# Kernel tuning notes

Measured on AMD Instinct MI355X. Metric: run time of the kernel, lower is better.

The kernel has to match this reference:

```python
import math
import jax, jax.numpy as jnp
import numpy as np

N_HEAD = 16
N_GROUPS = 32
EPS = 1e-05


def gelu(x):
    return 0.5 * x * (1.0 + jnp.tanh(math.sqrt(2.0 / math.pi) * (x + 0.044715 * x ** 3)))


def dp_group_norm(x, weight, bias, num_groups=N_GROUPS, eps=EPS):
    # x: [B, T, H]. torch F.group_norm on transposed [B, H, T] normalizes over
    # (channels_per_group, T) jointly per (batch, group).
    B, T, H = x.shape
    xg = x.reshape(B, T, num_groups, H // num_groups)
    mean = jnp.mean(xg, axis=(1, 3), keepdims=True)
    var = jnp.mean((xg - mean) ** 2, axis=(1, 3), keepdims=True)
    xn = ((xg - mean) / jnp.sqrt(var + eps)).reshape(B, T, H)
    return xn * weight + bias


def attention(x, w_attn, b_attn, w_aproj, b_aproj):
    B, T, H = x.shape
    hd = H // N_HEAD
    qkv = x @ w_attn + b_attn                      # [B, T, 3H]
    q, k, v = jnp.split(qkv, 3, axis=-1)
    q = q.reshape(B, T, N_HEAD, hd).transpose(0, 2, 1, 3)   # [B, nh, T, hd]
    k = k.reshape(B, T, N_HEAD, hd).transpose(0, 2, 1, 3)   # [B, nh, T, hd]
    v = v.reshape(B, T, N_HEAD, hd).transpose(0, 2, 1, 3)
    w = jnp.einsum('bhqd,bhkd->bhqk', q, k)        # no 1/sqrt(d): scale=False
    causal = jnp.tril(jnp.ones((T, T), dtype=x.dtype))
    w = w * causal - 1e10 * (1.0 - causal)
    w = jax.nn.softmax(w, axis=-1)
    a = jnp.einsum('bhqk,bhkd->bhqd', w, v)        # [B, nh, T, hd]
    a = a.transpose(0, 2, 1, 3).reshape(B, T, H)
    a = a @ w_aproj + b_aproj
    present = jnp.stack((k, v))                    # [2, B, nh, T, hd]
    return a, present


def setup_inputs() -> dict:
    key = jax.random.key(0)
    ks = jax.random.split(key, 6)
    B, T, H = 2, 2048, 1024
    return {
        'x': jax.random.normal(ks[0], (B, T, H), dtype=jnp.float32),
        'w_attn': jax.random.normal(ks[1], (H, 3 * H), dtype=jnp.float32) * 0.02,
        'b_attn': jnp.zeros((3 * H,), dtype=jnp.float32),
        'w_aproj': jax.random.normal(ks[2], (H, H), dtype=jnp.float32) * 0.02,
        'b_aproj': jnp.zeros((H,), dtype=jnp.float32),
        'ln1_w': jnp.ones((H,), dtype=jnp.float32),
        'ln1_b': jnp.zeros((H,), dtype=jnp.float32),
        'ln2_w': jnp.ones((H,), dtype=jnp.float32),
        'ln2_b': jnp.zeros((H,), dtype=jnp.float32),
        'w_fc': jax.random.normal(ks[3], (H, 4 * H), dtype=jnp.float32) * 0.02,
        'b_fc': jnp.zeros((4 * H,), dtype=jnp.float32),
        'w_mproj': jax.random.normal(ks[4], (4 * H, H), dtype=jnp.float32) * 0.02,
        'b_mproj': jnp.zeros((H,), dtype=jnp.float32),
    }


def reference(x, w_attn, b_attn, w_aproj, b_aproj, ln1_w, ln1_b, ln2_w, ln2_b,
              w_fc, b_fc, w_mproj, b_mproj):
    a, present = attention(dp_group_norm(x, ln1_w, ln1_b), w_attn, b_attn, w_aproj, b_aproj)
    x = x + a
    h = gelu(dp_group_norm(x, ln2_w, ln2_b) @ w_fc + b_fc)
    m = h @ w_mproj + b_mproj
    x = x + m
    return (x, present)
```

## Files before the change

kernel.cpp:

```cpp
#include <hip/hip_runtime.h>

#define B_  2
#define T_  2048
#define H_  1024
#define NH_ 16
#define HD_ 64
#define M_  (B_*T_)
#define PS_ 72

typedef __bf16 bf16x8 __attribute__((ext_vector_type(8)));
typedef float  floatx4 __attribute__((ext_vector_type(4)));

typedef __attribute__((address_space(1))) const unsigned int gas_u32;
typedef __attribute__((address_space(3))) unsigned int       las_u32;

__device__ __forceinline__ void gload_lds16(const __bf16* g, __bf16* l) {
    __builtin_amdgcn_global_load_lds((gas_u32*)g, (las_u32*)l, 16, 0, 0);
}

__global__ __launch_bounds__(256) void transpose_bf16(
    const float* __restrict__ in, __bf16* __restrict__ out, int K, int N)
{
    __shared__ float tile[32][33];
    const int k0 = blockIdx.x * 32, n0 = blockIdx.y * 32;
    const int tx = threadIdx.x & 31, ty = threadIdx.x >> 5;
#pragma unroll
    for (int i = 0; i < 32; i += 8)
        tile[ty + i][tx] = in[(size_t)(k0 + ty + i) * N + (n0 + tx)];
    __syncthreads();
#pragma unroll
    for (int i = 0; i < 32; i += 8)
        out[(size_t)(n0 + ty + i) * K + (k0 + tx)] = (__bf16)tile[tx][ty + i];
}

__global__ __launch_bounds__(256) void gn_partial(
    const float* __restrict__ x, float2* __restrict__ part)
{
    const int bg = blockIdx.x, chunk = blockIdx.y;
    const int batch = bg >> 5, g = bg & 31;
    const float* xp = x + (size_t)batch * T_ * H_ + g * 32;
    float s = 0.f, ss = 0.f;
    for (int i = threadIdx.x; i < 128 * 32; i += 256) {
        const int t = chunk * 128 + (i >> 5), c = i & 31;
        const float v = xp[(size_t)t * H_ + c];
        s += v; ss += v * v;
    }
#pragma unroll
    for (int off = 32; off > 0; off >>= 1) {
        s  += __shfl_down(s,  off, 64);
        ss += __shfl_down(ss, off, 64);
    }
    __shared__ float rs[4], rss[4];
    const int wv = threadIdx.x >> 6, lane = threadIdx.x & 63;
    if (lane == 0) { rs[wv] = s; rss[wv] = ss; }
    __syncthreads();
    if (threadIdx.x == 0)
        part[bg * 16 + chunk] =
            make_float2(rs[0] + rs[1] + rs[2] + rs[3],
                        rss[0] + rss[1] + rss[2] + rss[3]);
}

__global__ __launch_bounds__(64) void gn_finalize(
    const float2* __restrict__ part, float2* __restrict__ stats)
{
    const int bg = threadIdx.x;
    float s = 0.f, ss = 0.f;
#pragma unroll
    for (int i = 0; i < 16; ++i) {
        const float2 p = part[bg * 16 + i];
        s += p.x; ss += p.y;
    }
    const float inv = 1.f / (float)(T_ * 32);
    const float mean = s * inv;
    const float var  = ss * inv - mean * mean;
    stats[bg] = make_float2(mean, rsqrtf(var + 1e-5f));
}

__global__ __launch_bounds__(256) void gn_apply(
    const float* __restrict__ x, const float2* __restrict__ stats,
    const float* __restrict__ w, const float* __restrict__ bsc,
    __bf16* __restrict__ out)
{
    const size_t idx = ((size_t)blockIdx.x * 256 + threadIdx.x) * 4;
    const int h = (int)(idx & (H_ - 1));
    const int batch = (int)(idx >> 21);
    const float2 mr = stats[batch * 32 + (h >> 5)];
    const float4 xv = *(const float4*)(x + idx);
    const float4 wv = *(const float4*)(w + h);
    const float4 bv = *(const float4*)(bsc + h);
    __bf16 o[4];
    o[0] = (__bf16)((xv.x - mr.x) * mr.y * wv.x + bv.x);
    o[1] = (__bf16)((xv.y - mr.x) * mr.y * wv.y + bv.y);
    o[2] = (__bf16)((xv.z - mr.x) * mr.y * wv.z + bv.z);
    o[3] = (__bf16)((xv.w - mr.x) * mr.y * wv.w + bv.w);
    *(uint2*)(out + idx) = *(uint2*)o;
}

__device__ __forceinline__ void gemm_core(
    const __bf16* __restrict__ A, const __bf16* __restrict__ BT,
    int K, int m0, int n0, __bf16* As, __bf16* Bs, floatx4 (&acc)[4][4])
{
    const int tid  = threadIdx.x;
    const int lane = tid & 63, wv = tid >> 6;
    const int quad = lane >> 4, l16 = lane & 15;
    const int wm = (wv >> 1) * 64, wn = (wv & 1) * 64;
    const int r0 = tid >> 2, c0 = (tid & 3) * 8;

    const __bf16* Ag = A  + (size_t)(m0 + r0) * K + c0;
    const __bf16* Bg = BT + (size_t)(n0 + r0) * K + c0;

    for (int kt = 0; kt < K; kt += 64) {
        __syncthreads();
#pragma unroll
        for (int s = 0; s < 2; ++s) {
            gload_lds16(Ag + kt + s * 32,                As + s * 4096 + tid * 8);
            gload_lds16(Ag + (size_t)64 * K + kt + s * 32, As + s * 4096 + 2048 + tid * 8);
            gload_lds16(Bg + kt + s * 32,                Bs + s * 4096 + tid * 8);
            gload_lds16(Bg + (size_t)64 * K + kt + s * 32, Bs + s * 4096 + 2048 + tid * 8);
        }
        __syncthreads();
#pragma unroll
        for (int kk = 0; kk < 2; ++kk) {
            bf16x8 af[4], bfg[4];
#pragma unroll
            for (int i = 0; i < 4; ++i)
                af[i]  = *(const bf16x8*)(As + kk * 4096 + (wm + i * 16 + l16) * 32 + quad * 8);
#pragma unroll
            for (int i = 0; i < 4; ++i)
                bfg[i] = *(const bf16x8*)(Bs + kk * 4096 + (wn + i * 16 + l16) * 32 + quad * 8);
#pragma unroll
            for (int mi = 0; mi < 4; ++mi)
#pragma unroll
                for (int ni = 0; ni < 4; ++ni)
                    acc[mi][ni] = __builtin_amdgcn_mfma_f32_16x16x32_bf16(
                        af[mi], bfg[ni], acc[mi][ni], 0, 0, 0);
        }
    }
}

#define GEMM_PROLOGUE(KVAL)                                             \
    __shared__ __align__(16) __bf16 As[2 * 4096], Bs[2 * 4096];         \
    const int m0 = blockIdx.x * 128, n0 = blockIdx.y * 128;             \
    floatx4 acc[4][4];                                                  \
    { floatx4 z = {0.f, 0.f, 0.f, 0.f};                                 \
      for (int i = 0; i < 4; ++i) for (int j = 0; j < 4; ++j) acc[i][j] = z; } \
    gemm_core(A, BT, (KVAL), m0, n0, As, Bs, acc);                      \
    const int tid = threadIdx.x, lane = tid & 63, wv = tid >> 6;        \
    const int quad = lane >> 4, l16 = lane & 15;                        \
    const int wm = (wv >> 1) * 64, wn = (wv & 1) * 64;                  \
    (void)tid;

__global__ __launch_bounds__(256) void gemm_qkv(
    const __bf16* __restrict__ A, const __bf16* __restrict__ BT,
    const float* __restrict__ bias, __bf16* __restrict__ qb,
    __bf16* __restrict__ kb, __bf16* __restrict__ vtb,
    float* __restrict__ present)
{
    GEMM_PROLOGUE(H_)
#pragma unroll
    for (int ni = 0; ni < 4; ++ni) {
        const int col = n0 + wn + ni * 16 + l16;
        const float bv = bias[col];
        const int which = col >> 10, c = col & 1023, hh = c >> 6, d = c & 63;
#pragma unroll
        for (int mi = 0; mi < 4; ++mi)
#pragma unroll
            for (int r = 0; r < 4; ++r) {
                const int row = m0 + wm + mi * 16 + quad * 4 + r;
                const int bb = row >> 11, t = row & 2047;
                const float v = acc[mi][ni][r] + bv;
                const size_t idx = (((size_t)bb * NH_ + hh) * T_ + t) * HD_ + d;
                if (which == 0)      qb[idx] = (__bf16)v;
                else if (which == 1) { kb[idx] = (__bf16)v; present[idx] = v; }
                else { vtb[(((size_t)bb * NH_ + hh) * HD_ + d) * T_ + t] = (__bf16)v;
                       present[(size_t)B_ * NH_ * T_ * HD_ + idx] = v; }
            }
    }
}

__global__ __launch_bounds__(256) void gemm_gelu(
    const __bf16* __restrict__ A, const __bf16* __restrict__ BT,
    const float* __restrict__ bias, __bf16* __restrict__ out)
{
    GEMM_PROLOGUE(H_)
#pragma unroll
    for (int ni = 0; ni < 4; ++ni) {
        const int col = n0 + wn + ni * 16 + l16;
        const float bv = bias[col];
#pragma unroll
        for (int mi = 0; mi < 4; ++mi)
#pragma unroll
            for (int r = 0; r < 4; ++r) {
                const int row = m0 + wm + mi * 16 + quad * 4 + r;
                const float v = acc[mi][ni][r] + bv;
                const float g = 0.5f * v *
                    (1.f + tanhf(0.7978845608028654f * (v + 0.044715f * v * v * v)));
                out[(size_t)row * (4 * H_) + col] = (__bf16)g;
            }
    }
}

__global__ __launch_bounds__(256) void gemm_resid_n64(
    const __bf16* __restrict__ A, const __bf16* __restrict__ BT,
    const float* __restrict__ bias, const float* __restrict__ resid,
    float* __restrict__ out, int K, int N)
{
    __shared__ __align__(16) __bf16 As[2 * 4096], Bs[2 * 2048];
    const int m0 = blockIdx.x * 128, n0 = blockIdx.y * 64;
    const int tid  = threadIdx.x;
    const int lane = tid & 63, wv = tid >> 6;
    const int quad = lane >> 4, l16 = lane & 15;
    const int wm = (wv >> 1) * 64, wn = (wv & 1) * 32;
    const int r0 = tid >> 2, c0 = (tid & 3) * 8;

    floatx4 acc[4][2];
    { floatx4 z = {0.f, 0.f, 0.f, 0.f};
#pragma unroll
      for (int i = 0; i < 4; ++i) { acc[i][0] = z; acc[i][1] = z; } }

    const __bf16* Ag = A  + (size_t)(m0 + r0) * K + c0;
    const __bf16* Bg = BT + (size_t)(n0 + r0) * K + c0;

    for (int kt = 0; kt < K; kt += 64) {
        __syncthreads();
#pragma unroll
        for (int s = 0; s < 2; ++s) {
            gload_lds16(Ag + kt + s * 32,                  As + s * 4096 + tid * 8);
            gload_lds16(Ag + (size_t)64 * K + kt + s * 32, As + s * 4096 + 2048 + tid * 8);
            gload_lds16(Bg + kt + s * 32,                  Bs + s * 2048 + tid * 8);
        }
        __syncthreads();
#pragma unroll
        for (int kk = 0; kk < 2; ++kk) {
            bf16x8 af[4], bfg[2];
#pragma unroll
            for (int i = 0; i < 4; ++i)
                af[i]  = *(const bf16x8*)(As + kk * 4096 + (wm + i * 16 + l16) * 32 + quad * 8);
#pragma unroll
            for (int i = 0; i < 2; ++i)
                bfg[i] = *(const bf16x8*)(Bs + kk * 2048 + (wn + i * 16 + l16) * 32 + quad * 8);
#pragma unroll
            for (int mi = 0; mi < 4; ++mi)
#pragma unroll
                for (int ni = 0; ni < 2; ++ni)
                    acc[mi][ni] = __builtin_amdgcn_mfma_f32_16x16x32_bf16(
                        af[mi], bfg[ni], acc[mi][ni], 0, 0, 0);
        }
    }

#pragma unroll
    for (int ni = 0; ni < 2; ++ni) {
        const int col = n0 + wn + ni * 16 + l16;
        const float bv = bias[col];
#pragma unroll
        for (int mi = 0; mi < 4; ++mi)
#pragma unroll
            for (int r = 0; r < 4; ++r) {
                const int row = m0 + wm + mi * 16 + quad * 4 + r;
                const size_t idx = (size_t)row * N + col;
                out[idx] = acc[mi][ni][r] + bv + resid[idx];
            }
    }
}

__global__ __launch_bounds__(256) void attn_kernel(
    const __bf16* __restrict__ qb, const __bf16* __restrict__ kb,
    const __bf16* __restrict__ vtb, __bf16* __restrict__ aout)
{
    const int bh = blockIdx.x, pr = blockIdx.y;
    const int bb = bh >> 4, hh = bh & 15;
    const __bf16* Q  = qb  + (size_t)bh * T_ * HD_;
    const __bf16* Kp = kb  + (size_t)bh * T_ * HD_;
    const __bf16* VT = vtb + (size_t)bh * HD_ * T_;
    __shared__ __align__(16) __bf16 Qs[2 * 2048], Ks[2 * 2048], Vs[2 * 2048];
    __shared__ __align__(16) __bf16 Ps[64 * PS_];

    const int tid = threadIdx.x, lane = tid & 63, wv = tid >> 6;
    const int quad = lane >> 4, l16 = lane & 15;
    const int sr = tid >> 2, sc = (tid & 3) * 8;

    for (int half = 0; half < 2; ++half) {
        const int sp = half ? (31 - pr) : pr;
        const int q0 = sp * 64;
        const int nkt = sp + 1;

        __syncthreads();
#pragma unroll
        for (int s = 0; s < 2; ++s) {
            gload_lds16(Q  + (size_t)(q0 + sr) * HD_ + s * 32 + sc, Qs + s * 2048 + tid * 8);
            gload_lds16(Kp + (size_t)sr * HD_ + s * 32 + sc,        Ks + s * 2048 + tid * 8);
            gload_lds16(VT + (size_t)sr * T_  + s * 32 + sc,        Vs + s * 2048 + tid * 8);
        }

        float m_i[4], l_i[4];
        floatx4 Ov[4];
        { floatx4 z = {0.f, 0.f, 0.f, 0.f};
#pragma unroll
          for (int i = 0; i < 4; ++i) { Ov[i] = z; m_i[i] = -1e30f; l_i[i] = 0.f; } }

        for (int kt = 0; kt < nkt; ++kt) {
            __syncthreads();

            floatx4 sacc[4];
            { floatx4 z = {0.f, 0.f, 0.f, 0.f};
#pragma unroll
              for (int i = 0; i < 4; ++i) sacc[i] = z; }
#pragma unroll
            for (int kk = 0; kk < 2; ++kk) {
                const bf16x8 aq = *(const bf16x8*)(Qs + kk * 2048 + (wv * 16 + l16) * 32 + quad * 8);
#pragma unroll
                for (int ni = 0; ni < 4; ++ni) {
                    const bf16x8 bk = *(const bf16x8*)(Ks + kk * 2048 + (ni * 16 + l16) * 32 + quad * 8);
                    sacc[ni] = __builtin_amdgcn_mfma_f32_16x16x32_bf16(aq, bk, sacc[ni], 0, 0, 0);
                }
            }
            if (kt == sp) {
#pragma unroll
                for (int ni = 0; ni < 4; ++ni) {
                    const int keyL = ni * 16 + l16;
#pragma unroll
                    for (int r = 0; r < 4; ++r)
                        if (keyL > quad * 4 + r + wv * 16) sacc[ni][r] = -1e30f;
                }
            }
            float rmax[4], alpha[4], rsum[4];
#pragma unroll
            for (int r = 0; r < 4; ++r)
                rmax[r] = fmaxf(fmaxf(sacc[0][r], sacc[1][r]),
                                fmaxf(sacc[2][r], sacc[3][r]));
#pragma unroll
            for (int off = 1; off < 16; off <<= 1)
#pragma unroll
                for (int r = 0; r < 4; ++r)
                    rmax[r] = fmaxf(rmax[r], __shfl_xor(rmax[r], off, 64));
#pragma unroll
            for (int r = 0; r < 4; ++r) {
                const float mn = fmaxf(m_i[r], rmax[r]);
                alpha[r] = __expf(m_i[r] - mn);
                m_i[r] = mn;
                rsum[r] = 0.f;
            }
#pragma unroll
            for (int ni = 0; ni < 4; ++ni)
#pragma unroll
                for (int r = 0; r < 4; ++r) {
                    const float pe = __expf(sacc[ni][r] - m_i[r]);
                    sacc[ni][r] = pe;
                    rsum[r] += pe;
                }
#pragma unroll
            for (int off = 1; off < 16; off <<= 1)
#pragma unroll
                for (int r = 0; r < 4; ++r)
                    rsum[r] += __shfl_xor(rsum[r], off, 64);
#pragma unroll
            for (int r = 0; r < 4; ++r) {
                l_i[r] = l_i[r] * alpha[r] + rsum[r];
#pragma unroll
                for (int ni = 0; ni < 4; ++ni)
                    Ov[ni][r] *= alpha[r];
            }
#pragma unroll
            for (int ni = 0; ni < 4; ++ni)
#pragma unroll
                for (int r = 0; r < 4; ++r)
                    Ps[(wv * 16 + quad * 4 + r) * PS_ + ni * 16 + l16] = (__bf16)sacc[ni][r];
#pragma unroll
            for (int kk = 0; kk < 2; ++kk) {
                const bf16x8 ap = *(const bf16x8*)(Ps + (wv * 16 + l16) * PS_ + kk * 32 + quad * 8);
#pragma unroll
                for (int ni = 0; ni < 4; ++ni) {
                    const bf16x8 bv2 = *(const bf16x8*)(Vs + kk * 2048 + (ni * 16 + l16) * 32 + quad * 8);
                    Ov[ni] = __builtin_amdgcn_mfma_f32_16x16x32_bf16(ap, bv2, Ov[ni], 0, 0, 0);
                }
            }
            __syncthreads();
            if (kt + 1 < nkt) {
                const int kn = kt + 1;
#pragma unroll
                for (int s = 0; s < 2; ++s) {
                    gload_lds16(Kp + (size_t)(kn * 64 + sr) * HD_ + s * 32 + sc, Ks + s * 2048 + tid * 8);
                    gload_lds16(VT + (size_t)sr * T_ + kn * 64 + s * 32 + sc,    Vs + s * 2048 + tid * 8);
                }
            }
        }
#pragma unroll
        for (int ni = 0; ni < 4; ++ni)
#pragma unroll
            for (int r = 0; r < 4; ++r) {
                const int t = q0 + wv * 16 + quad * 4 + r;
                aout[((size_t)(bb * T_ + t)) * H_ + hh * HD_ + ni * 16 + l16] =
                    (__bf16)(Ov[ni][r] / l_i[r]);
            }
    }
}

extern "C" void kernel_launch(void* const* d_in, const int* in_sizes, int n_in,
                              void* d_out, int out_size, void* d_ws, size_t ws_size,
                              hipStream_t stream)
{
    (void)in_sizes; (void)n_in; (void)out_size; (void)ws_size;
    const float* x       = (const float*)d_in[0];
    const float* w_attn  = (const float*)d_in[1];
    const float* b_attn  = (const float*)d_in[2];
    const float* w_aproj = (const float*)d_in[3];
    const float* b_aproj = (const float*)d_in[4];
    const float* ln1_w   = (const float*)d_in[5];
    const float* ln1_b   = (const float*)d_in[6];
    const float* ln2_w   = (const float*)d_in[7];
    const float* ln2_b   = (const float*)d_in[8];
    const float* w_fc    = (const float*)d_in[9];
    const float* b_fc    = (const float*)d_in[10];
    const float* w_mproj = (const float*)d_in[11];
    const float* b_mproj = (const float*)d_in[12];
    float* out = (float*)d_out;
    float* present = out + (size_t)M_ * H_;

    char* wp = (char*)d_ws;
    auto alloc = [&](size_t bytes) {
        void* p = (void*)wp; wp += (bytes + 255) & ~(size_t)255; return p;
    };
    __bf16* A1       = (__bf16*)alloc((size_t)M_ * H_ * 2);
    __bf16* A2       = (__bf16*)alloc((size_t)M_ * H_ * 2);
    __bf16* WattnT   = (__bf16*)alloc((size_t)3 * H_ * H_ * 2);
    __bf16* WaprojT  = (__bf16*)alloc((size_t)H_ * H_ * 2);
    __bf16* WfcT     = (__bf16*)alloc((size_t)4 * H_ * H_ * 2);
    __bf16* WmprojT  = (__bf16*)alloc((size_t)4 * H_ * H_ * 2);
    __bf16* qb       = (__bf16*)alloc((size_t)M_ * H_ * 2);
    __bf16* kb       = (__bf16*)alloc((size_t)M_ * H_ * 2);
    __bf16* vtb      = (__bf16*)alloc((size_t)M_ * H_ * 2);
    __bf16* attn_out = (__bf16*)alloc((size_t)M_ * H_ * 2);
    float*  x2       = (float*) alloc((size_t)M_ * H_ * 4);
    __bf16* Hbuf     = (__bf16*)alloc((size_t)M_ * 4 * H_ * 2);
    float2* gn_part  = (float2*)alloc(64 * 16 * sizeof(float2));
    float2* gn_stats = (float2*)alloc(64 * sizeof(float2));

    transpose_bf16<<<dim3(H_/32, 3*H_/32), 256, 0, stream>>>(w_attn,  WattnT,  H_,   3*H_);
    transpose_bf16<<<dim3(H_/32, H_/32),   256, 0, stream>>>(w_aproj, WaprojT, H_,   H_);
    transpose_bf16<<<dim3(H_/32, 4*H_/32), 256, 0, stream>>>(w_fc,    WfcT,    H_,   4*H_);
    transpose_bf16<<<dim3(4*H_/32, H_/32), 256, 0, stream>>>(w_mproj, WmprojT, 4*H_, H_);

    gn_partial <<<dim3(64, 16), 256, 0, stream>>>(x, gn_part);
    gn_finalize<<<1, 64, 0, stream>>>(gn_part, gn_stats);
    gn_apply   <<<M_*H_/1024, 256, 0, stream>>>(x, gn_stats, ln1_w, ln1_b, A1);

    gemm_qkv<<<dim3(M_/128, 3*H_/128), 256, 0, stream>>>(A1, WattnT, b_attn,
                                                         qb, kb, vtb, present);
    attn_kernel<<<dim3(32, 16), 256, 0, stream>>>(qb, kb, vtb, attn_out);
    gemm_resid_n64<<<dim3(M_/128, H_/64), 256, 0, stream>>>(attn_out, WaprojT, b_aproj,
                                                            x, x2, H_, H_);

    gn_partial <<<dim3(64, 16), 256, 0, stream>>>(x2, gn_part);
    gn_finalize<<<1, 64, 0, stream>>>(gn_part, gn_stats);
    gn_apply   <<<M_*H_/1024, 256, 0, stream>>>(x2, gn_stats, ln2_w, ln2_b, A2);

    gemm_gelu<<<dim3(M_/128, 4*H_/128), 256, 0, stream>>>(A2, WfcT, b_fc, Hbuf);
    gemm_resid_n64<<<dim3(M_/128, H_/64), 256, 0, stream>>>(Hbuf, WmprojT, b_mproj,
                                                            x2, out, 4*H_, H_);
}
```

Baseline: 433.0 us.

## Double-buffer K/V in attention, swizzle LDS, use exp2 with lazy rescale

The attention kernel now double-buffers K/V tiles in LDS so the next tile's global-to-LDS load overlaps compute. It also XOR-swizzles the LDS layout to cut bank conflicts and keeps Q fragments in registers. It folds log2(e) into Q in the QKV GEMM so the softmax can use exp2, rescales the running max only when it grows by more than 8, and defers the row-sum reduction to the end. The grid changes from paired query blocks per CTA to one CTA per block, ordered longest-first. Risks include numerical drift from the lazy rescale in bf16 and more LDS use per CTA.

```diff
diff --git a/kernel.cpp b/kernel.cpp
--- a/kernel.cpp
+++ b/kernel.cpp
@@ -170,7 +170,7 @@
                 const int bb = row >> 11, t = row & 2047;
                 const float v = acc[mi][ni][r] + bv;
                 const size_t idx = (((size_t)bb * NH_ + hh) * T_ + t) * HD_ + d;
-                if (which == 0)      qb[idx] = (__bf16)v;
+                if (which == 0)      qb[idx] = (__bf16)(v * 1.4426950408889634f);
                 else if (which == 1) { kb[idx] = (__bf16)v; present[idx] = v; }
                 else { vtb[(((size_t)bb * NH_ + hh) * HD_ + d) * T_ + t] = (__bf16)v;
                        present[(size_t)B_ * NH_ * T_ * HD_ + idx] = v; }
@@ -267,132 +267,151 @@
     const __bf16* __restrict__ qb, const __bf16* __restrict__ kb,
     const __bf16* __restrict__ vtb, __bf16* __restrict__ aout)
 {
-    const int bh = blockIdx.x, pr = blockIdx.y;
+    const int bh = blockIdx.x;
+    const int sp = 31 - blockIdx.y;
     const int bb = bh >> 4, hh = bh & 15;
     const __bf16* Q  = qb  + (size_t)bh * T_ * HD_;
     const __bf16* Kp = kb  + (size_t)bh * T_ * HD_;
     const __bf16* VT = vtb + (size_t)bh * HD_ * T_;
-    __shared__ __align__(16) __bf16 Qs[2 * 2048], Ks[2 * 2048], Vs[2 * 2048];
+    __shared__ __align__(16) __bf16 Qs[2 * 2048];
+    __shared__ __align__(16) __bf16 Ks[2][2 * 2048];
+    __shared__ __align__(16) __bf16 Vs[2][2 * 2048];
     __shared__ __align__(16) __bf16 Ps[64 * PS_];
 
     const int tid = threadIdx.x, lane = tid & 63, wv = tid >> 6;
     const int quad = lane >> 4, l16 = lane & 15;
-    const int sr = tid >> 2, sc = (tid & 3) * 8;
-
-    for (int half = 0; half < 2; ++half) {
-        const int sp = half ? (31 - pr) : pr;
-        const int q0 = sp * 64;
-        const int nkt = sp + 1;
-
-        __syncthreads();
-#pragma unroll
-        for (int s = 0; s < 2; ++s) {
-            gload_lds16(Q  + (size_t)(q0 + sr) * HD_ + s * 32 + sc, Qs + s * 2048 + tid * 8);
-            gload_lds16(Kp + (size_t)sr * HD_ + s * 32 + sc,        Ks + s * 2048 + tid * 8);
-            gload_lds16(VT + (size_t)sr * T_  + s * 32 + sc,        Vs + s * 2048 + tid * 8);
-        }
-
-        float m_i[4], l_i[4];
-        floatx4 Ov[4];
+    const int sr = tid >> 2;
+    const int scs = (((tid & 3) ^ ((sr >> 1) & 3)) * 8);
+    const int xq8 = (quad ^ ((l16 >> 1) & 3)) * 8;
+
+    const int q0 = sp * 64, nkt = sp + 1;
+
+#pragma unroll
+    for (int s = 0; s < 2; ++s) {
+        gload_lds16(Q  + (size_t)(q0 + sr) * HD_ + s * 32 + scs, Qs + s * 2048 + tid * 8);
+        gload_lds16(Kp + (size_t)sr * HD_ + s * 32 + scs, &Ks[0][s * 2048 + tid * 8]);
+        gload_lds16(VT + (size_t)sr * T_  + s * 32 + scs, &Vs[0][s * 2048 + tid * 8]);
+    }
+    asm volatile("s_waitcnt vmcnt(0)" ::: "memory");
+    __builtin_amdgcn_s_barrier();
+    __builtin_amdgcn_sched_barrier(0);
+
+    bf16x8 aq[2];
+#pragma unroll
+    for (int kk = 0; kk < 2; ++kk)
+        aq[kk] = *(const bf16x8*)(Qs + kk * 2048 + (wv * 16 + l16) * 32 + xq8);
+
+    float m_i[4], l_p[4];
+    floatx4 Ov[4];
+    { floatx4 z = {0.f, 0.f, 0.f, 0.f};
+#pragma unroll
+      for (int i = 0; i < 4; ++i) { Ov[i] = z; m_i[i] = -1e30f; l_p[i] = 0.f; } }
+
+    int cur = 0;
+    for (int kt = 0; kt < nkt; ++kt) {
+        if (kt + 1 < nkt) {
+            const int kn = (kt + 1) * 64;
+#pragma unroll
+            for (int s = 0; s < 2; ++s) {
+                gload_lds16(Kp + (size_t)(kn + sr) * HD_ + s * 32 + scs,
+                            &Ks[cur ^ 1][s * 2048 + tid * 8]);
+                gload_lds16(VT + (size_t)sr * T_ + kn + s * 32 + scs,
+                            &Vs[cur ^ 1][s * 2048 + tid * 8]);
+            }
+            asm volatile("s_waitcnt vmcnt(4)" ::: "memory");
+        } else {
+            asm volatile("s_waitcnt vmcnt(0)" ::: "memory");
+        }
+        __builtin_amdgcn_s_barrier();
+        __builtin_amdgcn_sched_barrier(0);
+
+        const __bf16* Kc = Ks[cur];
+        const __bf16* Vc = Vs[cur];
+
+        floatx4 sacc[4];
         { floatx4 z = {0.f, 0.f, 0.f, 0.f};
 #pragma unroll
-          for (int i = 0; i < 4; ++i) { Ov[i] = z; m_i[i] = -1e30f; l_i[i] = 0.f; } }
-
-        for (int kt = 0; kt < nkt; ++kt) {
-            __syncthreads();
-
-            floatx4 sacc[4];
-            { floatx4 z = {0.f, 0.f, 0.f, 0.f};
-#pragma unroll
-              for (int i = 0; i < 4; ++i) sacc[i] = z; }
-#pragma unroll
-            for (int kk = 0; kk < 2; ++kk) {
-                const bf16x8 aq = *(const bf16x8*)(Qs + kk * 2048 + (wv * 16 + l16) * 32 + quad * 8);
-#pragma unroll
-                for (int ni = 0; ni < 4; ++ni) {
-                    const bf16x8 bk = *(const bf16x8*)(Ks + kk * 2048 + (ni * 16 + l16) * 32 + quad * 8);
-                    sacc[ni] = __builtin_amdgcn_mfma_f32_16x16x32_bf16(aq, bk, sacc[ni], 0, 0, 0);
-                }
-            }
-            if (kt == sp) {
-#pragma unroll
-                for (int ni = 0; ni < 4; ++ni) {
-                    const int keyL = ni * 16 + l16;
-#pragma unroll
-                    for (int r = 0; r < 4; ++r)
-                        if (keyL > quad * 4 + r + wv * 16) sacc[ni][r] = -1e30f;
-                }
-            }
-            float rmax[4], alpha[4], rsum[4];
+          for (int i = 0; i < 4; ++i) sacc[i] = z; }
+#pragma unroll
+        for (int kk = 0; kk < 2; ++kk)
+#pragma unroll
+            for (int ni = 0; ni < 4; ++ni) {
+                const bf16x8 bk = *(const bf16x8*)(Kc + kk * 2048 + (ni * 16 + l16) * 32 + xq8);
+                sacc[ni] = __builtin_amdgcn_mfma_f32_16x16x32_bf16(aq[kk], bk, sacc[ni], 0, 0, 0);
+            }
+        if (kt == sp) {
+#pragma unroll
+            for (int ni = 0; ni < 4; ++ni) {
+                const int keyL = ni * 16 + l16;
+#pragma unroll
+                for (int r = 0; r < 4; ++r)
+                    if (keyL > quad * 4 + r + wv * 16) sacc[ni][r] = -1e30f;
+            }
+        }
+        float rmax[4];
+#pragma unroll
+        for (int r = 0; r < 4; ++r)
+            rmax[r] = fmaxf(fmaxf(sacc[0][r], sacc[1][r]),
+                            fmaxf(sacc[2][r], sacc[3][r]));
+#pragma unroll
+        for (int off = 1; off < 16; off <<= 1)
 #pragma unroll
             for (int r = 0; r < 4; ++r)
-                rmax[r] = fmaxf(fmaxf(sacc[0][r], sacc[1][r]),
-                                fmaxf(sacc[2][r], sacc[3][r]));
-#pragma unroll
-            for (int off = 1; off < 16; off <<= 1)
-#pragma unroll
-                for (int r = 0; r < 4; ++r)
-                    rmax[r] = fmaxf(rmax[r], __shfl_xor(rmax[r], off, 64));
+                rmax[r] = fmaxf(rmax[r], __shfl_xor(rmax[r], off, 64));
+        float need = rmax[0] - m_i[0];
+#pragma unroll
+        for (int r = 1; r < 4; ++r) need = fmaxf(need, rmax[r] - m_i[r]);
+        if (__any(need > 8.f)) {
 #pragma unroll
             for (int r = 0; r < 4; ++r) {
                 const float mn = fmaxf(m_i[r], rmax[r]);
-                alpha[r] = __expf(m_i[r] - mn);
+                const float al = exp2f(m_i[r] - mn);
                 m_i[r] = mn;
-                rsum[r] = 0.f;
-            }
-#pragma unroll
-            for (int ni = 0; ni < 4; ++ni)
-#pragma unroll
-                for (int r = 0; r < 4; ++r) {
-                    const float pe = __expf(sacc[ni][r] - m_i[r]);
-                    sacc[ni][r] = pe;
-                    rsum[r] += pe;
-                }
-#pragma unroll
-            for (int off = 1; off < 16; off <<= 1)
-#pragma unroll
-                for (int r = 0; r < 4; ++r)
-                    rsum[r] += __shfl_xor(rsum[r], off, 64);
+                l_p[r] *= al;
+#pragma unroll
+                for (int ni = 0; ni < 4; ++ni) Ov[ni][r] *= al;
+            }
+        }
+#pragma unroll
+        for (int ni = 0; ni < 4; ++ni)
 #pragma unroll
             for (int r = 0; r < 4; ++r) {
-                l_i[r] = l_i[r] * alpha[r] + rsum[r];
-#pragma unroll
-                for (int ni = 0; ni < 4; ++ni)
-                    Ov[ni][r] *= alpha[r];
-            }
-#pragma unroll
-            for (int ni = 0; ni < 4; ++ni)
-#pragma unroll
-                for (int r = 0; r < 4; ++r)
-                    Ps[(wv * 16 + quad * 4 + r) * PS_ + ni * 16 + l16] = (__bf16)sacc[ni][r];
-#pragma unroll
-            for (int kk = 0; kk < 2; ++kk) {
-                const bf16x8 ap = *(const bf16x8*)(Ps + (wv * 16 + l16) * PS_ + kk * 32 + quad * 8);
-#pragma unroll
-                for (int ni = 0; ni < 4; ++ni) {
-                    const bf16x8 bv2 = *(const bf16x8*)(Vs + kk * 2048 + (ni * 16 + l16) * 32 + quad * 8);
-                    Ov[ni] = __builtin_amdgcn_mfma_f32_16x16x32_bf16(ap, bv2, Ov[ni], 0, 0, 0);
-                }
-            }
-            __syncthreads();
-            if (kt + 1 < nkt) {
-                const int kn = kt + 1;
-#pragma unroll
-                for (int s = 0; s < 2; ++s) {
-                    gload_lds16(Kp + (size_t)(kn * 64 + sr) * HD_ + s * 32 + sc, Ks + s * 2048 + tid * 8);
-                    gload_lds16(VT + (size_t)sr * T_ + kn * 64 + s * 32 + sc,    Vs + s * 2048 + tid * 8);
-                }
-            }
-        }
+                const float pe = exp2f(sacc[ni][r] - m_i[r]);
+                sacc[ni][r] = pe;
+                l_p[r] += pe;
+            }
 #pragma unroll
         for (int ni = 0; ni < 4; ++ni)
 #pragma unroll
-            for (int r = 0; r < 4; ++r) {
-                const int t = q0 + wv * 16 + quad * 4 + r;
-                aout[((size_t)(bb * T_ + t)) * H_ + hh * HD_ + ni * 16 + l16] =
-                    (__bf16)(Ov[ni][r] / l_i[r]);
-            }
-    }
+            for (int r = 0; r < 4; ++r)
+                Ps[(wv * 16 + quad * 4 + r) * PS_ + ni * 16 + l16] = (__bf16)sacc[ni][r];
+#pragma unroll
+        for (int kk = 0; kk < 2; ++kk) {
+            const bf16x8 ap = *(const bf16x8*)(Ps + (wv * 16 + l16) * PS_ + kk * 32 + quad * 8);
+#pragma unroll
+            for (int ni = 0; ni < 4; ++ni) {
+                const bf16x8 bv2 = *(const bf16x8*)(Vc + kk * 2048 + (ni * 16 + l16) * 32 + xq8);
+                Ov[ni] = __builtin_amdgcn_mfma_f32_16x16x32_bf16(ap, bv2, Ov[ni], 0, 0, 0);
+            }
+        }
+        __builtin_amdgcn_sched_barrier(0);
+        __builtin_amdgcn_s_barrier();
+        __builtin_amdgcn_sched_barrier(0);
+        cur ^= 1;
+    }
+#pragma unroll
+    for (int off = 1; off < 16; off <<= 1)
+#pragma unroll
+        for (int r = 0; r < 4; ++r)
+            l_p[r] += __shfl_xor(l_p[r], off, 64);
+#pragma unroll
+    for (int ni = 0; ni < 4; ++ni)
+#pragma unroll
+        for (int r = 0; r < 4; ++r) {
+            const int t = q0 + wv * 16 + quad * 4 + r;
+            aout[((size_t)(bb * T_ + t)) * H_ + hh * HD_ + ni * 16 + l16] =
+                (__bf16)(Ov[ni][r] / l_p[r]);
+        }
 }
 
 extern "C" void kernel_launch(void* const* d_in, const int* in_sizes, int n_in,
@@ -446,7 +465,7 @@
 
     gemm_qkv<<<dim3(M_/128, 3*H_/128), 256, 0, stream>>>(A1, WattnT, b_attn,
                                                          qb, kb, vtb, present);
-    attn_kernel<<<dim3(32, 16), 256, 0, stream>>>(qb, kb, vtb, attn_out);
+    attn_kernel<<<dim3(32, 32), 256, 0, stream>>>(qb, kb, vtb, attn_out);
     gemm_resid_n64<<<dim3(M_/128, H_/64), 256, 0, stream>>>(attn_out, WaprojT, b_aproj,
                                                             x, x2, H_, H_);
 
```

Measured after the change: 419.9 us. 1.03x faster.
